# Kernel optimization log

Hardware: AMD Instinct MI355X
Metric: run time of the kernel (lower is better)

## Reference

```python
import jax, jax.numpy as jnp
import numpy as np

EMB, VOCAB, HID, STY = 512, 32000, 1024, 512
B, L = 32, 64

def setup_inputs() -> dict:
    key = jax.random.key(0)
    ks = jax.random.split(key, 16)
    s = 0.02  # small init to keep gates unsaturated
    return {
        'rnn_inputs': jax.random.randint(ks[0], (B, L), 0, VOCAB),
        'sentence_vector': jax.random.normal(ks[1], (B, HID), dtype=jnp.float32) * 0.1,
        'embed': jax.random.normal(ks[2], (VOCAB, EMB), dtype=jnp.float32) * s,
        'U_w': jax.random.normal(ks[3], (EMB, 4 * STY), dtype=jnp.float32) * s,
        'U_b': jnp.zeros((4 * STY,), dtype=jnp.float32),
        'S1_w': jax.random.normal(ks[4], (4 * STY, STY), dtype=jnp.float32) * s,
        'S1_b': jnp.zeros((STY,), dtype=jnp.float32),
        'V_w': jax.random.normal(ks[5], (STY, 4 * HID), dtype=jnp.float32) * s,
        'V_b': jnp.zeros((4 * HID,), dtype=jnp.float32),
        'W_w': jax.random.normal(ks[6], (HID, 4 * HID), dtype=jnp.float32) * s,
        'W_b': jnp.zeros((4 * HID,), dtype=jnp.float32),
        'P_w': jax.random.normal(ks[7], (HID, VOCAB), dtype=jnp.float32) * s,
        'P_b': jnp.zeros((VOCAB,), dtype=jnp.float32),
    }

def reference(rnn_inputs, sentence_vector, embed, U_w, U_b, S1_w, S1_b,
              V_w, V_b, W_w, W_b, P_w, P_b):
    emb = embed[rnn_inputs]                     # [B, L, E]
    xs = jnp.swapaxes(emb[:, :-1, :], 0, 1)     # time-major [L-1, B, E]
    h0 = sentence_vector
    c0 = sentence_vector

    def step(carry, x):
        h, c = carry
        U = x @ U_w + U_b                       # [B, 4*STY]
        S = U @ S1_w + S1_b                     # [B, STY]  (mode='default')
        g = (S @ V_w + V_b) + (h @ W_w + W_b)   # [B, 4*HID]
        i, f, o, cg = jnp.split(g, 4, axis=1)   # split order i, f, o, c
        c_new = jax.nn.sigmoid(f) * c + jax.nn.sigmoid(i) * jnp.tanh(cg)
        h_new = jax.nn.sigmoid(o) * c_new
        out = h_new @ P_w + P_b                 # [B, VOCAB]
        return (h_new, c_new), out

    _, outs = jax.lax.scan(step, (h0, c0), xs)  # [L-1, B, VOCAB]
    return jnp.swapaxes(outs, 0, 1)             # [B, L-1, VOCAB]
```

## Files before the change

kernel.cpp:

```cpp
#include <hip/hip_runtime.h>
#include <hip/hip_bf16.h>


typedef __bf16 bf16;
typedef bf16 bf16x8 __attribute__((ext_vector_type(8)));
typedef float f32x4 __attribute__((ext_vector_type(4)));

#define NB 32
#define NL 64
#define NT 63
#define NE 512
#define NS4 2048
#define NS 512
#define NH 1024
#define NG 4096
#define NV 32000
#define MPAD 2048

__device__ __forceinline__ float sigmoidf_(float x) { return 1.0f / (1.0f + expf(-x)); }

__device__ __forceinline__ void gload_lds16(const bf16* g, bf16* l) {
  __builtin_amdgcn_global_load_lds(
      (const __attribute__((address_space(1))) unsigned int*)g,
      (__attribute__((address_space(3))) unsigned int*)l, 16, 0, 0);
}

__global__ void k_transpose_cvt(const float* __restrict__ src, bf16* __restrict__ dst,
                                int R, int C) {
  __shared__ float t[32][33];
  int bx = blockIdx.x * 32;
  int by = blockIdx.y * 32;
  int tx = threadIdx.x & 31, ty = threadIdx.x >> 5;
#pragma unroll
  for (int i = 0; i < 32; i += 8)
    t[ty + i][tx] = src[(size_t)(by + ty + i) * C + (bx + tx)];
  __syncthreads();
#pragma unroll
  for (int i = 0; i < 32; i += 8)
    dst[(size_t)(bx + ty + i) * R + (by + tx)] = (bf16)t[tx][ty + i];
}

__global__ void k_gather(const int* __restrict__ rnn, const float* __restrict__ embed,
                         bf16* __restrict__ X) {
  int r = blockIdx.x;
  if (r < NB * NT) {
    int t = r >> 5, b = r & 31;
    int tok = rnn[b * NL + t];
    const float* src = embed + (size_t)tok * NE;
    for (int e = threadIdx.x; e < NE; e += 256) X[(size_t)r * NE + e] = (bf16)src[e];
  } else {
    for (int e = threadIdx.x; e < NE; e += 256) X[(size_t)r * NE + e] = (bf16)0.0f;
  }
}

__global__ void k_init(const float* __restrict__ sv, bf16* __restrict__ h0,
                       unsigned* __restrict__ bar) {
  int i = blockIdx.x * 256 + threadIdx.x;
  if (i == 0) *bar = 0u;
  if (i < NB * NH) h0[i] = (bf16)sv[i];
}

__global__ void k_bias2(const float* __restrict__ a, const float* __restrict__ b,
                        float* __restrict__ o) {
  int i = blockIdx.x * 256 + threadIdx.x;
  if (i < NG) o[i] = a[i] + b[i];
}

template <int OUT_MODE>
__global__ __launch_bounds__(256, 2) void k_gemm(const bf16* __restrict__ A,
                                                 const bf16* __restrict__ Bt,
                                                 const float* __restrict__ bias,
                                                 void* __restrict__ Cp, int K, int N) {
  __shared__ bf16 As[128 * 32];
  __shared__ bf16 Bs[128 * 32];
  const int tid = threadIdx.x;
  const int m0 = blockIdx.y * 128, n0 = blockIdx.x * 128;
  const int lane = tid & 63, w = tid >> 6;
  const int l15 = lane & 15, kq = lane >> 4;
  const int m_off = (w & 1) * 64, n_off = (w >> 1) * 64;
  const int c0 = 2 * w, c1 = 2 * w + 1;
  const int sub = lane >> 2, kkl = (lane & 3) * 8;
  const bf16* pA0 = A + (size_t)(m0 + c0 * 16 + sub) * K + kkl;
  const bf16* pA1 = A + (size_t)(m0 + c1 * 16 + sub) * K + kkl;
  const bf16* pB0 = Bt + (size_t)(n0 + c0 * 16 + sub) * K + kkl;
  const bf16* pB1 = Bt + (size_t)(n0 + c1 * 16 + sub) * K + kkl;
  f32x4 acc[4][4] = {};
  for (int k0 = 0; k0 < K; k0 += 32) {
    __syncthreads();
    gload_lds16(pA0 + k0, &As[c0 * 512]);
    gload_lds16(pA1 + k0, &As[c1 * 512]);
    gload_lds16(pB0 + k0, &Bs[c0 * 512]);
    gload_lds16(pB1 + k0, &Bs[c1 * 512]);
    __syncthreads();
    bf16x8 a[4], b[4];
#pragma unroll
    for (int i = 0; i < 4; i++)
      a[i] = *(const bf16x8*)&As[(m_off + 16 * i + l15) * 32 + kq * 8];
#pragma unroll
    for (int j = 0; j < 4; j++)
      b[j] = *(const bf16x8*)&Bs[(n_off + 16 * j + l15) * 32 + kq * 8];
#pragma unroll
    for (int i = 0; i < 4; i++)
#pragma unroll
      for (int j = 0; j < 4; j++)
        acc[i][j] = __builtin_amdgcn_mfma_f32_16x16x32_bf16(a[i], b[j], acc[i][j], 0, 0, 0);
  }
#pragma unroll
  for (int j = 0; j < 4; j++) {
    const int col = n0 + n_off + 16 * j + l15;
    const float bv = bias[col];
#pragma unroll
    for (int i = 0; i < 4; i++) {
#pragma unroll
      for (int r = 0; r < 4; r++) {
        const int row = m0 + m_off + 16 * i + kq * 4 + r;
        const float v = acc[i][j][r] + bv;
        if (OUT_MODE == 0) {
          ((bf16*)Cp)[(size_t)row * N + col] = (bf16)v;
        } else if (OUT_MODE == 1) {
          ((float*)Cp)[(size_t)row * N + col] = v;
        } else {
          if (row < NB * NT) {
            int t = row >> 5, b = row & 31;
            ((float*)Cp)[((size_t)b * NT + t) * NV + col] = v;
          }
        }
      }
    }
  }
}

__global__ __launch_bounds__(256, 1) void k_rnn(const bf16* __restrict__ Wt,
                                                const float* __restrict__ Gx,
                                                const float* __restrict__ sv,
                                                bf16* __restrict__ hb,
                                                unsigned* __restrict__ bar) {
  __shared__ bf16 hs[16 * 1032];
  __shared__ float gl[4][16][16];
  __shared__ float cs[16][16];
  const int tid = threadIdx.x;
  const int lane = tid & 63, g = tid >> 6;
  const int l15 = lane & 15, kq = lane >> 4;
  const int cg = blockIdx.x >> 1;
  const int bh = blockIdx.x & 1;
  const int j0 = cg * 16;
  const int brow0 = bh * 16;
  const int bb_e = tid >> 4, jj_e = tid & 15;
  cs[bb_e][jj_e] = sv[(brow0 + bb_e) * NH + j0 + jj_e];
  const bf16* wrow = Wt + (size_t)(g * NH + j0 + l15) * NH;
  bf16x8 breg[32];
#pragma unroll
  for (int k = 0; k < 32; k++) breg[k] = *(const bf16x8*)&wrow[k * 32 + kq * 8];
  unsigned target = 0;
  for (int t = 0; t < NT; t++) {
    const bf16* hp = hb + (size_t)t * NB * NH + (size_t)brow0 * NH;
    __syncthreads();
#pragma unroll
    for (int q = 0; q < 8; q++) {
      int idx = tid + 256 * q;
      int row = idx >> 7, col = (idx & 127) * 8;
      *(bf16x8*)&hs[row * 1032 + col] = *(const bf16x8*)&hp[row * NH + col];
    }
    __syncthreads();
    f32x4 acc = {};
#pragma unroll
    for (int k = 0; k < 32; k++) {
      bf16x8 a = *(const bf16x8*)&hs[l15 * 1032 + k * 32 + kq * 8];
      acc = __builtin_amdgcn_mfma_f32_16x16x32_bf16(a, breg[k], acc, 0, 0, 0);
    }
#pragma unroll
    for (int r = 0; r < 4; r++) gl[g][kq * 4 + r][l15] = acc[r];
    __syncthreads();
    {
      const int j = j0 + jj_e;
      const float* gx = Gx + (size_t)t * NB * NG + (size_t)(brow0 + bb_e) * NG;
      float gi = gl[0][bb_e][jj_e] + gx[j];
      float gf = gl[1][bb_e][jj_e] + gx[NH + j];
      float go = gl[2][bb_e][jj_e] + gx[2 * NH + j];
      float gc = gl[3][bb_e][jj_e] + gx[3 * NH + j];
      float cp = cs[bb_e][jj_e];
      float cn = sigmoidf_(gf) * cp + sigmoidf_(gi) * tanhf(gc);
      float hn = sigmoidf_(go) * cn;
      cs[bb_e][jj_e] = cn;
      hb[(size_t)(t + 1) * NB * NH + (size_t)(brow0 + bb_e) * NH + j] = (bf16)hn;
    }
    if (t + 1 < NT) {
      target += gridDim.x;
      __syncthreads();
      if (tid == 0) {
        __hip_atomic_fetch_add(bar, 1u, __ATOMIC_ACQ_REL, __HIP_MEMORY_SCOPE_AGENT);
        while (__hip_atomic_load(bar, __ATOMIC_ACQUIRE, __HIP_MEMORY_SCOPE_AGENT) <
               target)
          __builtin_amdgcn_s_sleep(2);
      }
      __syncthreads();
    }
  }
}

extern "C" void kernel_launch(void* const* d_in, const int* in_sizes, int n_in,
                              void* d_out, int out_size, void* d_ws, size_t ws_size,
                              hipStream_t stream) {
  const int* rnn = (const int*)d_in[0];
  const float* sv = (const float*)d_in[1];
  const float* embed = (const float*)d_in[2];
  const float* U_w = (const float*)d_in[3];
  const float* U_b = (const float*)d_in[4];
  const float* S1_w = (const float*)d_in[5];
  const float* S1_b = (const float*)d_in[6];
  const float* V_w = (const float*)d_in[7];
  const float* V_b = (const float*)d_in[8];
  const float* W_w = (const float*)d_in[9];
  const float* W_b = (const float*)d_in[10];
  const float* P_w = (const float*)d_in[11];
  const float* P_b = (const float*)d_in[12];
  float* out = (float*)d_out;

  char* ws = (char*)d_ws;
  size_t off = 0;
  auto alloc = [&](size_t bytes) -> void* {
    void* p = ws + off;
    off += (bytes + 255) & ~(size_t)255;
    return p;
  };
  bf16* Pt = (bf16*)alloc((size_t)NV * NH * 2);
  float* Gx = (float*)alloc((size_t)MPAD * NG * 4);
  bf16* Ub = (bf16*)alloc((size_t)MPAD * NS4 * 2);
  bf16* Wt = (bf16*)alloc((size_t)NG * NH * 2);
  bf16* hb = (bf16*)alloc((size_t)(MPAD + 32) * NH * 2);
  bf16* Vt = (bf16*)alloc((size_t)NG * NS * 2);
  bf16* Xb = (bf16*)alloc((size_t)MPAD * NE * 2);
  bf16* Ut = (bf16*)alloc((size_t)NS4 * NE * 2);
  bf16* S1t = (bf16*)alloc((size_t)NS * NS4 * 2);
  bf16* Sb = (bf16*)alloc((size_t)MPAD * NS * 2);
  float* vbwb = (float*)alloc((size_t)NG * 4);
  unsigned* bar = (unsigned*)alloc(256);
  (void)in_sizes; (void)n_in; (void)out_size; (void)ws_size;

  k_transpose_cvt<<<dim3(NS4 / 32, NE / 32), 256, 0, stream>>>(U_w, Ut, NE, NS4);
  k_transpose_cvt<<<dim3(NS / 32, NS4 / 32), 256, 0, stream>>>(S1_w, S1t, NS4, NS);
  k_transpose_cvt<<<dim3(NG / 32, NS / 32), 256, 0, stream>>>(V_w, Vt, NS, NG);
  k_transpose_cvt<<<dim3(NG / 32, NH / 32), 256, 0, stream>>>(W_w, Wt, NH, NG);
  k_transpose_cvt<<<dim3(NV / 32, NH / 32), 256, 0, stream>>>(P_w, Pt, NH, NV);
  k_bias2<<<NG / 256, 256, 0, stream>>>(V_b, W_b, vbwb);
  k_init<<<(NB * NH + 255) / 256, 256, 0, stream>>>(sv, hb, bar);
  k_gather<<<MPAD, 256, 0, stream>>>(rnn, embed, Xb);

  k_gemm<0><<<dim3(NS4 / 128, MPAD / 128), 256, 0, stream>>>(Xb, Ut, U_b, Ub, NE, NS4);
  k_gemm<0><<<dim3(NS / 128, MPAD / 128), 256, 0, stream>>>(Ub, S1t, S1_b, Sb, NS4, NS);
  k_gemm<1><<<dim3(NG / 128, MPAD / 128), 256, 0, stream>>>(Sb, Vt, vbwb, Gx, NS, NG);

  k_rnn<<<128, 256, 0, stream>>>(Wt, Gx, sv, hb, bar);

  k_gemm<2><<<dim3(NV / 128, MPAD / 128), 256, 0, stream>>>(hb + (size_t)NB * NH, Pt,
                                                            P_b, out, NH, NV);
}
```

Before: 1.136 ms.

## Shrink recurrent kernel to 32 blocks with per-block flag barrier

The recurrent LSTM kernel now runs on 32 blocks of 512 threads instead of 128 blocks of 256. Each block covers 32 hidden units for all 32 batch rows, so each wave does two MFMA chains that share the same W fragment. The single atomic-counter grid barrier becomes per-block padded flags, which one wave polls together with a wave-wide all-check. The Gx gate inputs are also prefetched into registers before the h load. Fewer blocks and flag-based sync should cut per-step barrier latency, but each block now does more work per step and fewer CUs are active.

```diff
diff --git a/kernel.cpp b/kernel.cpp
--- a/kernel.cpp
+++ b/kernel.cpp
@@ -17,6 +17,9 @@
 #define NV 32000
 #define MPAD 2048
 
+#define RNB 32
+#define FSTR 32
+
 __device__ __forceinline__ float sigmoidf_(float x) { return 1.0f / (1.0f + expf(-x)); }
 
 __device__ __forceinline__ void gload_lds16(const bf16* g, bf16* l) {
@@ -54,9 +57,9 @@
 }
 
 __global__ void k_init(const float* __restrict__ sv, bf16* __restrict__ h0,
-                       unsigned* __restrict__ bar) {
+                       unsigned* __restrict__ flags) {
   int i = blockIdx.x * 256 + threadIdx.x;
-  if (i == 0) *bar = 0u;
+  if (i < RNB * FSTR) flags[i] = 0u;
   if (i < NB * NH) h0[i] = (bf16)sv[i];
 }
 
@@ -130,68 +133,88 @@
   }
 }
 
-__global__ __launch_bounds__(256, 1) void k_rnn(const bf16* __restrict__ Wt,
-                                                const float* __restrict__ Gx,
-                                                const float* __restrict__ sv,
-                                                bf16* __restrict__ hb,
-                                                unsigned* __restrict__ bar) {
-  __shared__ bf16 hs[16 * 1032];
-  __shared__ float gl[4][16][16];
-  __shared__ float cs[16][16];
+__global__ __launch_bounds__(512) void k_rnn(const bf16* __restrict__ Wt,
+                                             const float* __restrict__ Gx,
+                                             const float* __restrict__ sv,
+                                             bf16* __restrict__ hb,
+                                             unsigned* __restrict__ flags) {
+  __shared__ bf16 hs[32 * 1032];
+  __shared__ float gl[4][32][32];
+  __shared__ float cs[32][32];
   const int tid = threadIdx.x;
-  const int lane = tid & 63, g = tid >> 6;
+  const int lane = tid & 63, wid = tid >> 6;
+  const int g = wid & 3, ch = wid >> 2;
   const int l15 = lane & 15, kq = lane >> 4;
-  const int cg = blockIdx.x >> 1;
-  const int bh = blockIdx.x & 1;
-  const int j0 = cg * 16;
-  const int brow0 = bh * 16;
+  const int j0 = blockIdx.x * 32;
   const int bb_e = tid >> 4, jj_e = tid & 15;
-  cs[bb_e][jj_e] = sv[(brow0 + bb_e) * NH + j0 + jj_e];
-  const bf16* wrow = Wt + (size_t)(g * NH + j0 + l15) * NH;
+
+  cs[bb_e][jj_e] = sv[bb_e * NH + j0 + jj_e];
+  cs[bb_e][jj_e + 16] = sv[bb_e * NH + j0 + jj_e + 16];
+
+  const bf16* wrow = Wt + (size_t)(g * NH + j0 + ch * 16 + l15) * NH;
   bf16x8 breg[32];
 #pragma unroll
   for (int k = 0; k < 32; k++) breg[k] = *(const bf16x8*)&wrow[k * 32 + kq * 8];
-  unsigned target = 0;
+
   for (int t = 0; t < NT; t++) {
-    const bf16* hp = hb + (size_t)t * NB * NH + (size_t)brow0 * NH;
-    __syncthreads();
+    const float* gx0 = Gx + (size_t)t * NB * NG + (size_t)bb_e * NG + j0;
+    float gxr[8];
+#pragma unroll
+    for (int u = 0; u < 2; u++)
+#pragma unroll
+      for (int gg = 0; gg < 4; gg++)
+        gxr[u * 4 + gg] = gx0[gg * NH + jj_e + u * 16];
+    const bf16* hp = hb + (size_t)t * NB * NH;
 #pragma unroll
     for (int q = 0; q < 8; q++) {
-      int idx = tid + 256 * q;
+      int idx = tid + 512 * q;
       int row = idx >> 7, col = (idx & 127) * 8;
       *(bf16x8*)&hs[row * 1032 + col] = *(const bf16x8*)&hp[row * NH + col];
     }
     __syncthreads();
-    f32x4 acc = {};
+    f32x4 acc0 = {}, acc1 = {};
 #pragma unroll
     for (int k = 0; k < 32; k++) {
-      bf16x8 a = *(const bf16x8*)&hs[l15 * 1032 + k * 32 + kq * 8];
-      acc = __builtin_amdgcn_mfma_f32_16x16x32_bf16(a, breg[k], acc, 0, 0, 0);
-    }
-#pragma unroll
-    for (int r = 0; r < 4; r++) gl[g][kq * 4 + r][l15] = acc[r];
-    __syncthreads();
-    {
-      const int j = j0 + jj_e;
-      const float* gx = Gx + (size_t)t * NB * NG + (size_t)(brow0 + bb_e) * NG;
-      float gi = gl[0][bb_e][jj_e] + gx[j];
-      float gf = gl[1][bb_e][jj_e] + gx[NH + j];
-      float go = gl[2][bb_e][jj_e] + gx[2 * NH + j];
-      float gc = gl[3][bb_e][jj_e] + gx[3 * NH + j];
-      float cp = cs[bb_e][jj_e];
+      bf16x8 a0 = *(const bf16x8*)&hs[l15 * 1032 + k * 32 + kq * 8];
+      bf16x8 a1 = *(const bf16x8*)&hs[(16 + l15) * 1032 + k * 32 + kq * 8];
+      acc0 = __builtin_amdgcn_mfma_f32_16x16x32_bf16(a0, breg[k], acc0, 0, 0, 0);
+      acc1 = __builtin_amdgcn_mfma_f32_16x16x32_bf16(a1, breg[k], acc1, 0, 0, 0);
+    }
+#pragma unroll
+    for (int r = 0; r < 4; r++) {
+      gl[g][kq * 4 + r][ch * 16 + l15] = acc0[r];
+      gl[g][16 + kq * 4 + r][ch * 16 + l15] = acc1[r];
+    }
+    __syncthreads();
+    bf16* hw = hb + (size_t)(t + 1) * NB * NH + (size_t)bb_e * NH + j0;
+#pragma unroll
+    for (int u = 0; u < 2; u++) {
+      const int jj = jj_e + u * 16;
+      float gi = gl[0][bb_e][jj] + gxr[u * 4 + 0];
+      float gf = gl[1][bb_e][jj] + gxr[u * 4 + 1];
+      float go = gl[2][bb_e][jj] + gxr[u * 4 + 2];
+      float gc = gl[3][bb_e][jj] + gxr[u * 4 + 3];
+      float cp = cs[bb_e][jj];
       float cn = sigmoidf_(gf) * cp + sigmoidf_(gi) * tanhf(gc);
       float hn = sigmoidf_(go) * cn;
-      cs[bb_e][jj_e] = cn;
-      hb[(size_t)(t + 1) * NB * NH + (size_t)(brow0 + bb_e) * NH + j] = (bf16)hn;
+      cs[bb_e][jj] = cn;
+      hw[jj] = (bf16)hn;
     }
     if (t + 1 < NT) {
-      target += gridDim.x;
       __syncthreads();
-      if (tid == 0) {
-        __hip_atomic_fetch_add(bar, 1u, __ATOMIC_ACQ_REL, __HIP_MEMORY_SCOPE_AGENT);
-        while (__hip_atomic_load(bar, __ATOMIC_ACQUIRE, __HIP_MEMORY_SCOPE_AGENT) <
-               target)
-          __builtin_amdgcn_s_sleep(2);
+      if (wid == 0) {
+        __builtin_amdgcn_fence(__ATOMIC_RELEASE, "agent");
+        if (lane == 0)
+          __hip_atomic_store(&flags[blockIdx.x * FSTR], (unsigned)(t + 1),
+                             __ATOMIC_RELAXED, __HIP_MEMORY_SCOPE_AGENT);
+        const unsigned tgt = (unsigned)(t + 1);
+        for (;;) {
+          unsigned v = __hip_atomic_load(&flags[(lane & 31) * FSTR],
+                                         __ATOMIC_RELAXED, __HIP_MEMORY_SCOPE_AGENT);
+          if (__all((int)(v >= tgt))) break;
+          __builtin_amdgcn_s_sleep(1);
+        }
+        __builtin_amdgcn_fence(__ATOMIC_ACQUIRE, "agent");
       }
       __syncthreads();
     }
@@ -234,7 +257,7 @@
   bf16* S1t = (bf16*)alloc((size_t)NS * NS4 * 2);
   bf16* Sb = (bf16*)alloc((size_t)MPAD * NS * 2);
   float* vbwb = (float*)alloc((size_t)NG * 4);
-  unsigned* bar = (unsigned*)alloc(256);
+  unsigned* flags = (unsigned*)alloc((size_t)RNB * FSTR * 4);
   (void)in_sizes; (void)n_in; (void)out_size; (void)ws_size;
 
   k_transpose_cvt<<<dim3(NS4 / 32, NE / 32), 256, 0, stream>>>(U_w, Ut, NE, NS4);
@@ -243,14 +266,14 @@
   k_transpose_cvt<<<dim3(NG / 32, NH / 32), 256, 0, stream>>>(W_w, Wt, NH, NG);
   k_transpose_cvt<<<dim3(NV / 32, NH / 32), 256, 0, stream>>>(P_w, Pt, NH, NV);
   k_bias2<<<NG / 256, 256, 0, stream>>>(V_b, W_b, vbwb);
-  k_init<<<(NB * NH + 255) / 256, 256, 0, stream>>>(sv, hb, bar);
+  k_init<<<(NB * NH + 255) / 256, 256, 0, stream>>>(sv, hb, flags);
   k_gather<<<MPAD, 256, 0, stream>>>(rnn, embed, Xb);
 
   k_gemm<0><<<dim3(NS4 / 128, MPAD / 128), 256, 0, stream>>>(Xb, Ut, U_b, Ub, NE, NS4);
   k_gemm<0><<<dim3(NS / 128, MPAD / 128), 256, 0, stream>>>(Ub, S1t, S1_b, Sb, NS4, NS);
   k_gemm<1><<<dim3(NG / 128, MPAD / 128), 256, 0, stream>>>(Sb, Vt, vbwb, Gx, NS, NG);
 
-  k_rnn<<<128, 256, 0, stream>>>(Wt, Gx, sv, hb, bar);
+  k_rnn<<<RNB, 512, 0, stream>>>(Wt, Gx, sv, hb, flags);
 
   k_gemm<2><<<dim3(NV / 128, MPAD / 128), 256, 0, stream>>>(hb + (size_t)NB * NH, Pt,
                                                             P_b, out, NH, NV);
```

Measured after the change: 1.040 ms. 8.5% less time.
